# Kernel tuning notes

Measured on AMD Instinct MI355X. Metric: run time of the kernel, lower is better.

The kernel has to match this reference:

```python
import jax, jax.numpy as jnp
import numpy as np

N, E = 40000, 640000
IN_DIM, EDGE_DIM, HID = 128, 64, 128


def setup_inputs() -> dict:
    key = jax.random.key(0)
    ks = jax.random.split(key, 10)
    x = jax.random.normal(ks[0], (N, IN_DIM), dtype=jnp.float32)
    edge_index = jax.random.randint(ks[1], (2, E), 0, N, dtype=jnp.int64)
    edge_attr = jax.random.normal(ks[2], (E, EDGE_DIM), dtype=jnp.float32)
    # learned params (xavier-ish scaling)
    Wh_w = jax.random.normal(ks[3], (EDGE_DIM, HID), dtype=jnp.float32) / np.sqrt(EDGE_DIM)
    Wh_b = jnp.zeros((HID,), dtype=jnp.float32)
    Wn_w = jax.random.normal(ks[4], (2 * IN_DIM, HID), dtype=jnp.float32) / np.sqrt(2 * IN_DIM)
    Wn_b = jnp.zeros((HID,), dtype=jnp.float32)
    w_e = jax.random.normal(ks[5], (HID, 1), dtype=jnp.float32) / np.sqrt(HID)
    ft_w = jax.random.normal(ks[6], (IN_DIM, IN_DIM), dtype=jnp.float32) / np.sqrt(IN_DIM)
    ft_b = jnp.zeros((IN_DIM,), dtype=jnp.float32)
    return {"x": x, "edge_index": edge_index, "edge_attr": edge_attr,
            "Wh_w": Wh_w, "Wh_b": Wh_b, "Wn_w": Wn_w, "Wn_b": Wn_b,
            "w_e": w_e, "ft_w": ft_w, "ft_b": ft_b}


def reference(x, edge_index, edge_attr, Wh_w, Wh_b, Wn_w, Wn_b, w_e, ft_w, ft_b):
    src, dst = edge_index[0], edge_index[1]
    # gather endpoint features and run edge MLP: relu(W_h(e) + W_n([x_src; x_dst]))
    node_feat = jnp.concatenate([x[src], x[dst]], axis=1)          # [E, 2*in_dim]
    edge_h = edge_attr @ Wh_w + Wh_b                               # [E, hid]
    node_h = node_feat @ Wn_w + Wn_b                               # [E, hid]
    combined = jax.nn.relu(edge_h + node_h)
    scores = (combined @ w_e)[:, 0]                                # [E]
    alpha = jax.nn.softmax(scores, axis=0)                         # softmax over all edges
    # scatter-add weighted dst features into src nodes (same-type branch)
    local = jnp.zeros_like(x).at[src].add(-alpha[:, None] * x[dst])
    out = x + local
    out = out + out @ ft_w + ft_b
    return out
```

## Files before the change

### kernel.cpp

```cpp
#include <hip/hip_runtime.h>
#include <math.h>

#define N_NODES 40000
#define E_EDGES 640000
#define IN_DIM 128
#define EDGE_DIM 64
#define HID 128
#define EB 10000
#define NPART (EB * 4)

typedef unsigned int u32;
typedef unsigned short u16;
typedef __attribute__((ext_vector_type(4))) float f32x4;
typedef __attribute__((ext_vector_type(8))) short bf16x8;

__device__ __forceinline__ float bf_lo(u32 d) { return __uint_as_float(d << 16); }
__device__ __forceinline__ float bf_hi(u32 d) { return __uint_as_float(d & 0xffff0000u); }
__device__ __forceinline__ u16 f2bf(float f) {
    u32 u = __float_as_uint(f);
    return (u16)((u + 0x7fffu + ((u >> 16) & 1u)) >> 16);
}
__device__ __forceinline__ u32 pack_bf(float lo, float hi) {
    return ((u32)f2bf(hi) << 16) | (u32)f2bf(lo);
}


__global__ __launch_bounds__(256) void k_pre(const float* __restrict__ x,
                                             const float* __restrict__ Whw,
                                             const float* __restrict__ Wnw,
                                             const float* __restrict__ ftw,
                                             const int* __restrict__ eidx,
                                             u16* __restrict__ xb,
                                             u32* __restrict__ counts,
                                             u16* __restrict__ Whtb,
                                             u16* __restrict__ WnAT,
                                             u16* __restrict__ WnBT,
                                             u16* __restrict__ fttb) {
    if (blockIdx.x < 20000) {
        int i = blockIdx.x * 256 + threadIdx.x;
        xb[i] = f2bf(x[i]);
    } else if (blockIdx.x < 20224) {
        int i = (blockIdx.x - 20000) * 256 + threadIdx.x;
        if (i < 8192) {
            int h = i >> 6, k = i & 63;
            Whtb[i] = f2bf(Whw[k * HID + h]);
        } else if (i < 24576) {
            int j = i - 8192, h = j >> 7, k = j & 127;
            WnAT[j] = f2bf(Wnw[k * HID + h]);
        } else if (i < 40960) {
            int j = i - 24576, h = j >> 7, k = j & 127;
            WnBT[j] = f2bf(Wnw[(IN_DIM + k) * HID + h]);
        } else {
            int j = i - 40960, h = j >> 7, k = j & 127;
            fttb[j] = f2bf(ftw[k * IN_DIM + h]);
        }
    } else {
        int e = (blockIdx.x - 20224) * 256 + threadIdx.x;
        atomicAdd(&counts[eidx[e]], 1u);
    }
}

__global__ __launch_bounds__(256) void k_proj(const u16* __restrict__ xb,
                                              const u16* __restrict__ WnAT,
                                              const u16* __restrict__ WnBT,
                                              const float* __restrict__ Whb,
                                              const float* __restrict__ Wnb,
                                              u16* __restrict__ P1b,
                                              u16* __restrict__ P2b) {
    const int t = threadIdx.x, w = t >> 6, lane = t & 63;
    const int mrow = lane & 15, quad = lane >> 4;
    const int rowBase = blockIdx.x * 64 + w * 16;

    bf16x8 a[4];
    const u16* ar = xb + (size_t)(rowBase + mrow) * IN_DIM + quad * 8;
#pragma unroll
    for (int ks = 0; ks < 4; ++ks) a[ks] = *(const bf16x8*)(ar + ks * 32);

#pragma unroll
    for (int nt = 0; nt < 8; ++nt) {
        const u16* b1p = WnAT + (size_t)(nt * 16 + mrow) * IN_DIM + quad * 8;
        const u16* b2p = WnBT + (size_t)(nt * 16 + mrow) * IN_DIM + quad * 8;
        f32x4 c1 = {0.f, 0.f, 0.f, 0.f}, c2 = {0.f, 0.f, 0.f, 0.f};
#pragma unroll
        for (int ks = 0; ks < 4; ++ks) {
            c1 = __builtin_amdgcn_mfma_f32_16x16x32_bf16(a[ks], *(const bf16x8*)(b1p + ks * 32), c1, 0, 0, 0);
            c2 = __builtin_amdgcn_mfma_f32_16x16x32_bf16(a[ks], *(const bf16x8*)(b2p + ks * 32), c2, 0, 0, 0);
        }
        const int col = nt * 16 + mrow;
        const float bias = Whb[col] + Wnb[col];
#pragma unroll
        for (int r = 0; r < 4; ++r) {
            int row = rowBase + quad * 4 + r;
            P1b[(size_t)row * HID + col] = f2bf(c1[r] + bias);
            P2b[(size_t)row * HID + col] = f2bf(c2[r]);
        }
    }
}

__global__ __launch_bounds__(1024) void k_scan(const u32* __restrict__ counts,
                                               u32* __restrict__ off,
                                               u32* __restrict__ cur) {
    __shared__ u32 sums[1024];
    const int t = threadIdx.x;
    const int CH = 40;
    u32 local[CH];
    u32 s = 0;
    const int base = t * CH;
#pragma unroll
    for (int i = 0; i < CH; ++i) {
        int idx = base + i;
        u32 c = (idx < N_NODES) ? counts[idx] : 0u;
        local[i] = s;
        s += c;
    }
    sums[t] = s;
    __syncthreads();
    for (int o = 1; o < 1024; o <<= 1) {
        u32 v = (t >= o) ? sums[t - o] : 0u;
        __syncthreads();
        sums[t] += v;
        __syncthreads();
    }
    const u32 pre = sums[t] - s;
#pragma unroll
    for (int i = 0; i < CH; ++i) {
        int idx = base + i;
        if (idx < N_NODES) {
            u32 v = pre + local[i];
            off[idx] = v;
            cur[idx] = v;
        }
    }
    if (t == 1023) off[N_NODES] = sums[1023];
}

__global__ __launch_bounds__(256) void k_edge(const int* __restrict__ eidx,
                                              const float* __restrict__ ea,
                                              const u16* __restrict__ Whtb,
                                              const u16* __restrict__ P1b,
                                              const u16* __restrict__ P2b,
                                              const float* __restrict__ we,
                                              u32* __restrict__ cur,
                                              uint2* __restrict__ sde,
                                              float* __restrict__ partials) {
    __shared__ u32 Psp[4][16][68];
    const int t = threadIdx.x, w = t >> 6, lane = t & 63;
    const int e0 = blockIdx.x * 64 + w * 16;
    const int mrow = lane & 15, quad = lane >> 4;

    const int m = lane >> 2, c4 = lane & 3;
    const int srcm = eidx[e0 + m];
    const int dstm = eidx[E_EDGES + e0 + m];
    const uint4* p1 = (const uint4*)(P1b + (size_t)srcm * HID + c4 * 32);
    const uint4* p2 = (const uint4*)(P2b + (size_t)dstm * HID + c4 * 32);
    uint4 pa[4], pb[4];
#pragma unroll
    for (int i = 0; i < 4; ++i) { pa[i] = p1[i]; pb[i] = p2[i]; }

    const float* arow = ea + (size_t)(e0 + mrow) * EDGE_DIM + quad * 8;
    float4 f0 = *(const float4*)(arow);
    float4 f1 = *(const float4*)(arow + 4);
    float4 f2 = *(const float4*)(arow + 32);
    float4 f3 = *(const float4*)(arow + 36);

#pragma unroll
    for (int i = 0; i < 4; ++i) {
        u32 da[4] = {pa[i].x, pa[i].y, pa[i].z, pa[i].w};
        u32 db[4] = {pb[i].x, pb[i].y, pb[i].z, pb[i].w};
        uint4 o;
        o.x = pack_bf(bf_lo(da[0]) + bf_lo(db[0]), bf_hi(da[0]) + bf_hi(db[0]));
        o.y = pack_bf(bf_lo(da[1]) + bf_lo(db[1]), bf_hi(da[1]) + bf_hi(db[1]));
        o.z = pack_bf(bf_lo(da[2]) + bf_lo(db[2]), bf_hi(da[2]) + bf_hi(db[2]));
        o.w = pack_bf(bf_lo(da[3]) + bf_lo(db[3]), bf_hi(da[3]) + bf_hi(db[3]));
        *(uint4*)&Psp[w][m][c4 * 16 + i * 4] = o;
    }

    bf16x8 a0, a1;
    a0[0] = (short)f2bf(f0.x); a0[1] = (short)f2bf(f0.y);
    a0[2] = (short)f2bf(f0.z); a0[3] = (short)f2bf(f0.w);
    a0[4] = (short)f2bf(f1.x); a0[5] = (short)f2bf(f1.y);
    a0[6] = (short)f2bf(f1.z); a0[7] = (short)f2bf(f1.w);
    a1[0] = (short)f2bf(f2.x); a1[1] = (short)f2bf(f2.y);
    a1[2] = (short)f2bf(f2.z); a1[3] = (short)f2bf(f2.w);
    a1[4] = (short)f2bf(f3.x); a1[5] = (short)f2bf(f3.y);
    a1[6] = (short)f2bf(f3.z); a1[7] = (short)f2bf(f3.w);

    float wsum[4] = {0.f, 0.f, 0.f, 0.f};
    const u16* bbase = Whtb + (size_t)mrow * EDGE_DIM + quad * 8;
#pragma unroll
    for (int nt = 0; nt < 8; ++nt) {
        const u16* bp = bbase + nt * 16 * EDGE_DIM;
        bf16x8 b0 = *(const bf16x8*)(bp);
        bf16x8 b1 = *(const bf16x8*)(bp + 32);
        f32x4 c = {0.f, 0.f, 0.f, 0.f};
        c = __builtin_amdgcn_mfma_f32_16x16x32_bf16(a0, b0, c, 0, 0, 0);
        c = __builtin_amdgcn_mfma_f32_16x16x32_bf16(a1, b1, c, 0, 0, 0);
        float wv = we[nt * 16 + mrow];
#pragma unroll
        for (int r = 0; r < 4; ++r) {
            u32 u = Psp[w][quad * 4 + r][nt * 8 + (mrow >> 1)];
            float p = (mrow & 1) ? bf_hi(u) : bf_lo(u);
            wsum[r] += fmaxf(c[r] + p, 0.f) * wv;
        }
    }

#pragma unroll
    for (int off = 1; off < 16; off <<= 1) {
#pragma unroll
        for (int r = 0; r < 4; ++r) wsum[r] += __shfl_xor(wsum[r], off, 16);
    }
    float ex[4]; float s4 = 0.f;
#pragma unroll
    for (int r = 0; r < 4; ++r) { ex[r] = __expf(wsum[r]); s4 += ex[r]; }

    if (mrow == 0) {
#pragma unroll
        for (int r = 0; r < 4; ++r) {
            int e = e0 + quad * 4 + r;
            int s = eidx[e];
            int d = eidx[E_EDGES + e];
            u32 pos = atomicAdd(&cur[s], 1u);
            sde[pos] = make_uint2((u32)d, __float_as_uint(-ex[r]));
        }
    }

    s4 += __shfl_xor(s4, 16, 64);
    s4 += __shfl_xor(s4, 32, 64);
    if (lane == 0) partials[blockIdx.x * 4 + w] = s4;
}

__global__ __launch_bounds__(256) void k_accum(const u32* __restrict__ off,
                                               const uint2* __restrict__ sde,
                                               const float* __restrict__ partials,
                                               float* __restrict__ sumExp,
                                               const u16* __restrict__ xb,
                                               float* __restrict__ out) {
    if (blockIdx.x == 0) {
        float s = 0.f;
        for (int i = threadIdx.x; i < NPART; i += 256) s += partials[i];
#pragma unroll
        for (int o = 1; o < 64; o <<= 1) s += __shfl_xor(s, o, 64);
        __shared__ float ws4[4];
        if ((threadIdx.x & 63) == 0) ws4[threadIdx.x >> 6] = s;
        __syncthreads();
        if (threadIdx.x == 0) sumExp[0] = ws4[0] + ws4[1] + ws4[2] + ws4[3];
        return;
    }
    const int lane = threadIdx.x & 63;
    const int n = (blockIdx.x - 1) * 4 + (threadIdx.x >> 6);
    const u32 o0 = off[n], o1 = off[n + 1];

    float acc0 = 0.f, acc1 = 0.f;
    for (u32 base = o0; base < o1; base += 64) {
        u32 j = base + (u32)lane;
        uint2 dv = make_uint2(0u, 0u);
        if (j < o1) dv = sde[j];
        int cnt = (int)min(64u, o1 - base);
        int jj = 0;
        for (; jj + 8 <= cnt; jj += 8) {
            u32 d[8]; float a[8]; u32 q[8];
#pragma unroll
            for (int k = 0; k < 8; ++k) {
                d[k] = __shfl(dv.x, jj + k, 64);
                a[k] = __uint_as_float(__shfl(dv.y, jj + k, 64));
            }
#pragma unroll
            for (int k = 0; k < 8; ++k)
                q[k] = ((const u32*)(xb + (size_t)d[k] * IN_DIM))[lane];
#pragma unroll
            for (int k = 0; k < 8; ++k) {
                acc0 = fmaf(a[k], bf_lo(q[k]), acc0);
                acc1 = fmaf(a[k], bf_hi(q[k]), acc1);
            }
        }
        for (; jj + 4 <= cnt; jj += 4) {
            u32 d[4]; float a[4]; u32 q[4];
#pragma unroll
            for (int k = 0; k < 4; ++k) {
                d[k] = __shfl(dv.x, jj + k, 64);
                a[k] = __uint_as_float(__shfl(dv.y, jj + k, 64));
            }
#pragma unroll
            for (int k = 0; k < 4; ++k)
                q[k] = ((const u32*)(xb + (size_t)d[k] * IN_DIM))[lane];
#pragma unroll
            for (int k = 0; k < 4; ++k) {
                acc0 = fmaf(a[k], bf_lo(q[k]), acc0);
                acc1 = fmaf(a[k], bf_hi(q[k]), acc1);
            }
        }
        for (; jj < cnt; ++jj) {
            u32 dst = __shfl(dv.x, jj, 64);
            float a = __uint_as_float(__shfl(dv.y, jj, 64));
            u32 q = ((const u32*)(xb + (size_t)dst * IN_DIM))[lane];
            acc0 = fmaf(a, bf_lo(q), acc0);
            acc1 = fmaf(a, bf_hi(q), acc1);
        }
    }
    float* op = out + (size_t)n * IN_DIM + 2 * lane;
    op[0] = acc0;
    op[1] = acc1;
}

__global__ __launch_bounds__(256) void k_final(const float* __restrict__ x,
                                               const u16* __restrict__ fttb,
                                               const float* __restrict__ ftb,
                                               const float* __restrict__ sumExp,
                                               float* __restrict__ out) {
    __shared__ u32 ybp[64][68];
    const float invS = 1.0f / sumExp[0];
    const int t = threadIdx.x;
    const int rb = blockIdx.x * 64;

    {
        const int rr = t >> 2, seg = t & 3;
        const float4* xp = (const float4*)(x + (size_t)(rb + rr) * IN_DIM + seg * 32);
        const float4* lp = (const float4*)(out + (size_t)(rb + rr) * IN_DIM + seg * 32);
#pragma unroll
        for (int i = 0; i < 4; ++i) {
            float4 xa = xp[2 * i], xc = xp[2 * i + 1];
            float4 la = lp[2 * i], lc = lp[2 * i + 1];
            uint4 o;
            o.x = pack_bf(fmaf(invS, la.x, xa.x), fmaf(invS, la.y, xa.y));
            o.y = pack_bf(fmaf(invS, la.z, xa.z), fmaf(invS, la.w, xa.w));
            o.z = pack_bf(fmaf(invS, lc.x, xc.x), fmaf(invS, lc.y, xc.y));
            o.w = pack_bf(fmaf(invS, lc.z, xc.z), fmaf(invS, lc.w, xc.w));
            *(uint4*)&ybp[rr][seg * 16 + i * 4] = o;
        }
    }
    __syncthreads();

    const int w = t >> 6, lane = t & 63;
    const int mrow = lane & 15, quad = lane >> 4;
    const int rowBase = rb + w * 16;

    bf16x8 a[4];
#pragma unroll
    for (int ks = 0; ks < 4; ++ks)
        a[ks] = *(const bf16x8*)&ybp[w * 16 + mrow][ks * 16 + quad * 4];

#pragma unroll
    for (int nt = 0; nt < 8; ++nt) {
        const u16* bp = fttb + (size_t)(nt * 16 + mrow) * IN_DIM + quad * 8;
        f32x4 c = {0.f, 0.f, 0.f, 0.f};
#pragma unroll
        for (int ks = 0; ks < 4; ++ks)
            c = __builtin_amdgcn_mfma_f32_16x16x32_bf16(a[ks], *(const bf16x8*)(bp + ks * 32), c, 0, 0, 0);
        const int col = nt * 16 + mrow;
        const float fb = ftb[col];
#pragma unroll
        for (int r = 0; r < 4; ++r) {
            int row = rowBase + quad * 4 + r;
            size_t idx = (size_t)row * IN_DIM + col;
            float y = fmaf(invS, out[idx], x[idx]);
            out[idx] = y + c[r] + fb;
        }
    }
}

extern "C" void kernel_launch(void* const* d_in, const int* in_sizes, int n_in,
                              void* d_out, int out_size, void* d_ws, size_t ws_size,
                              hipStream_t stream) {
    const float* x    = (const float*)d_in[0];
    const int*   eidx = (const int*)d_in[1];
    const float* ea   = (const float*)d_in[2];
    const float* Whw  = (const float*)d_in[3];
    const float* Whb  = (const float*)d_in[4];
    const float* Wnw  = (const float*)d_in[5];
    const float* Wnb  = (const float*)d_in[6];
    const float* we   = (const float*)d_in[7];
    const float* ftw  = (const float*)d_in[8];
    const float* ftb  = (const float*)d_in[9];
    float* out = (float*)d_out;

    uint2* sde      = (uint2*)d_ws;
    u16*   P1b      = (u16*)(sde + (size_t)E_EDGES);
    u16*   P2b      = P1b + (size_t)N_NODES * HID;
    u16*   xb       = P2b + (size_t)N_NODES * HID;
    u16*   Whtb     = xb + (size_t)N_NODES * IN_DIM;
    u16*   WnAT     = Whtb + (size_t)EDGE_DIM * HID;
    u16*   WnBT     = WnAT + (size_t)HID * IN_DIM;
    u16*   fttb     = WnBT + (size_t)HID * IN_DIM;
    float* partials = (float*)(fttb + (size_t)IN_DIM * IN_DIM);
    float* sumExp   = partials + NPART;
    u32*   counts   = (u32*)(sumExp + 1);
    u32*   off      = counts + N_NODES;
    u32*   cur      = off + N_NODES + 1;

    hipMemsetAsync(counts, 0, (size_t)N_NODES * sizeof(u32), stream);
    k_pre  <<<22724, 256, 0, stream>>>(x, Whw, Wnw, ftw, eidx, xb, counts,
                                       Whtb, WnAT, WnBT, fttb);
    k_scan <<<1, 1024, 0, stream>>>(counts, off, cur);
    k_proj <<<N_NODES / 64, 256, 0, stream>>>(xb, WnAT, WnBT, Whb, Wnb, P1b, P2b);
    k_edge <<<EB, 256, 0, stream>>>(eidx, ea, Whtb, P1b, P2b, we, cur, sde, partials);
    k_accum<<<N_NODES / 4 + 1, 256, 0, stream>>>(off, sde, partials, sumExp, xb, out);
    k_final<<<N_NODES / 64, 256, 0, stream>>>(x, fttb, ftb, sumExp, out);
}
```

Baseline: 550.7 us.

## Fold scan into projection kernel, hoist edge atomics, widen accumulate unroll

The single-block prefix-scan kernel is merged into the projection launch as an extra block that uses 256 threads with a sequential 157-element chunk per thread. This removes one launch and lets the scan run alongside the projection GEMM. In the edge kernel, the src/dst indices are fetched by shuffling values already loaded, and the atomicAdd on the cursor is issued early so its latency overlaps the MFMA work. The accumulate loop gathers 16 neighbour rows per step instead of 8, putting more loads in flight at the cost of more registers.

Result: slower. 577.9 us (+4.9%).

```diff
diff --git a/kernel.cpp b/kernel.cpp
--- a/kernel.cpp
+++ b/kernel.cpp
@@ -60,13 +60,47 @@
     }
 }
 
-__global__ __launch_bounds__(256) void k_proj(const u16* __restrict__ xb,
-                                              const u16* __restrict__ WnAT,
-                                              const u16* __restrict__ WnBT,
-                                              const float* __restrict__ Whb,
-                                              const float* __restrict__ Wnb,
-                                              u16* __restrict__ P1b,
-                                              u16* __restrict__ P2b) {
+__global__ __launch_bounds__(256) void k_projscan(const u16* __restrict__ xb,
+                                                  const u16* __restrict__ WnAT,
+                                                  const u16* __restrict__ WnBT,
+                                                  const float* __restrict__ Whb,
+                                                  const float* __restrict__ Wnb,
+                                                  u16* __restrict__ P1b,
+                                                  u16* __restrict__ P2b,
+                                                  const u32* __restrict__ counts,
+                                                  u32* __restrict__ off,
+                                                  u32* __restrict__ cur) {
+    if (blockIdx.x == 625) {
+        const int t = threadIdx.x;
+        const int CH = 157;
+        const int base = t * CH;
+        u32 s = 0;
+        for (int i = 0; i < CH; ++i) {
+            int idx = base + i;
+            if (idx < N_NODES) s += counts[idx];
+        }
+        __shared__ u32 sums[256];
+        sums[t] = s;
+        __syncthreads();
+        for (int o = 1; o < 256; o <<= 1) {
+            u32 v = (t >= o) ? sums[t - o] : 0u;
+            __syncthreads();
+            sums[t] += v;
+            __syncthreads();
+        }
+        u32 run = sums[t] - s;
+        for (int i = 0; i < CH; ++i) {
+            int idx = base + i;
+            if (idx < N_NODES) {
+                u32 c = counts[idx];
+                off[idx] = run;
+                cur[idx] = run;
+                run += c;
+            }
+        }
+        if (t == 255) off[N_NODES] = sums[255];
+        return;
+    }
     const int t = threadIdx.x, w = t >> 6, lane = t & 63;
     const int mrow = lane & 15, quad = lane >> 4;
     const int rowBase = blockIdx.x * 64 + w * 16;
@@ -95,43 +129,6 @@
             P2b[(size_t)row * HID + col] = f2bf(c2[r]);
         }
     }
-}
-
-__global__ __launch_bounds__(1024) void k_scan(const u32* __restrict__ counts,
-                                               u32* __restrict__ off,
-                                               u32* __restrict__ cur) {
-    __shared__ u32 sums[1024];
-    const int t = threadIdx.x;
-    const int CH = 40;
-    u32 local[CH];
-    u32 s = 0;
-    const int base = t * CH;
-#pragma unroll
-    for (int i = 0; i < CH; ++i) {
-        int idx = base + i;
-        u32 c = (idx < N_NODES) ? counts[idx] : 0u;
-        local[i] = s;
-        s += c;
-    }
-    sums[t] = s;
-    __syncthreads();
-    for (int o = 1; o < 1024; o <<= 1) {
-        u32 v = (t >= o) ? sums[t - o] : 0u;
-        __syncthreads();
-        sums[t] += v;
-        __syncthreads();
-    }
-    const u32 pre = sums[t] - s;
-#pragma unroll
-    for (int i = 0; i < CH; ++i) {
-        int idx = base + i;
-        if (idx < N_NODES) {
-            u32 v = pre + local[i];
-            off[idx] = v;
-            cur[idx] = v;
-        }
-    }
-    if (t == 1023) off[N_NODES] = sums[1023];
 }
 
 __global__ __launch_bounds__(256) void k_edge(const int* __restrict__ eidx,
@@ -163,6 +160,17 @@
     float4 f2 = *(const float4*)(arow + 32);
     float4 f3 = *(const float4*)(arow + 36);
 
+    u32 sArr[4], dArr[4], pos[4];
+#pragma unroll
+    for (int r = 0; r < 4; ++r) {
+        sArr[r] = (u32)__shfl(srcm, (quad * 4 + r) << 2, 64);
+        dArr[r] = (u32)__shfl(dstm, (quad * 4 + r) << 2, 64);
+    }
+    if (mrow == 0) {
+#pragma unroll
+        for (int r = 0; r < 4; ++r) pos[r] = atomicAdd(&cur[sArr[r]], 1u);
+    }
+
 #pragma unroll
     for (int i = 0; i < 4; ++i) {
         u32 da[4] = {pa[i].x, pa[i].y, pa[i].z, pa[i].w};
@@ -215,13 +223,8 @@
 
     if (mrow == 0) {
 #pragma unroll
-        for (int r = 0; r < 4; ++r) {
-            int e = e0 + quad * 4 + r;
-            int s = eidx[e];
-            int d = eidx[E_EDGES + e];
-            u32 pos = atomicAdd(&cur[s], 1u);
-            sde[pos] = make_uint2((u32)d, __float_as_uint(-ex[r]));
-        }
+        for (int r = 0; r < 4; ++r)
+            sde[pos[r]] = make_uint2(dArr[r], __float_as_uint(-ex[r]));
     }
 
     s4 += __shfl_xor(s4, 16, 64);
@@ -257,18 +260,18 @@
         if (j < o1) dv = sde[j];
         int cnt = (int)min(64u, o1 - base);
         int jj = 0;
-        for (; jj + 8 <= cnt; jj += 8) {
-            u32 d[8]; float a[8]; u32 q[8];
-#pragma unroll
-            for (int k = 0; k < 8; ++k) {
+        for (; jj + 16 <= cnt; jj += 16) {
+            u32 d[16]; float a[16]; u32 q[16];
+#pragma unroll
+            for (int k = 0; k < 16; ++k) {
                 d[k] = __shfl(dv.x, jj + k, 64);
                 a[k] = __uint_as_float(__shfl(dv.y, jj + k, 64));
             }
 #pragma unroll
-            for (int k = 0; k < 8; ++k)
+            for (int k = 0; k < 16; ++k)
                 q[k] = ((const u32*)(xb + (size_t)d[k] * IN_DIM))[lane];
 #pragma unroll
-            for (int k = 0; k < 8; ++k) {
+            for (int k = 0; k < 16; ++k) {
                 acc0 = fmaf(a[k], bf_lo(q[k]), acc0);
                 acc1 = fmaf(a[k], bf_hi(q[k]), acc1);
             }
@@ -388,11 +391,11 @@
     u32*   cur      = off + N_NODES + 1;
 
     hipMemsetAsync(counts, 0, (size_t)N_NODES * sizeof(u32), stream);
-    k_pre  <<<22724, 256, 0, stream>>>(x, Whw, Wnw, ftw, eidx, xb, counts,
-                                       Whtb, WnAT, WnBT, fttb);
-    k_scan <<<1, 1024, 0, stream>>>(counts, off, cur);
-    k_proj <<<N_NODES / 64, 256, 0, stream>>>(xb, WnAT, WnBT, Whb, Wnb, P1b, P2b);
-    k_edge <<<EB, 256, 0, stream>>>(eidx, ea, Whtb, P1b, P2b, we, cur, sde, partials);
-    k_accum<<<N_NODES / 4 + 1, 256, 0, stream>>>(off, sde, partials, sumExp, xb, out);
-    k_final<<<N_NODES / 64, 256, 0, stream>>>(x, fttb, ftb, sumExp, out);
-}
+    k_pre     <<<22724, 256, 0, stream>>>(x, Whw, Wnw, ftw, eidx, xb, counts,
+                                          Whtb, WnAT, WnBT, fttb);
+    k_projscan<<<626, 256, 0, stream>>>(xb, WnAT, WnBT, Whb, Wnb, P1b, P2b,
+                                        counts, off, cur);
+    k_edge    <<<EB, 256, 0, stream>>>(eidx, ea, Whtb, P1b, P2b, we, cur, sde, partials);
+    k_accum   <<<N_NODES / 4 + 1, 256, 0, stream>>>(off, sde, partials, sumExp, xb, out);
+    k_final   <<<N_NODES / 64, 256, 0, stream>>>(x, fttb, ftb, sumExp, out);
+}
```
